# Kernel tuning notes

Measured on AMD Instinct MI355X. Metric: run time of the kernel, lower is better.

Reference implementation:

```python
import jax, jax.numpy as jnp
import numpy as np

T, H, F, E, K, C = 8192, 1024, 2048, 16, 2, 1280  # tokens, hidden, ffn, experts, top_k, capacity


def setup_inputs() -> dict:
    key = jax.random.key(0)
    ks = jax.random.split(key, 6)
    return {
        "x": jax.random.normal(ks[0], (T, H), dtype=jnp.float32),
        "w_router": jax.random.normal(ks[1], (H, E), dtype=jnp.float32) * 0.02,
        "w1": jax.random.normal(ks[2], (E, H, F), dtype=jnp.float32) * 0.02,
        "b1": jnp.zeros((E, F), dtype=jnp.float32),
        "w2": jax.random.normal(ks[3], (E, F, H), dtype=jnp.float32) * 0.02,
        "b2": jnp.zeros((E, H), dtype=jnp.float32),
    }


def reference(x, w_router, w1, b1, w2, b2):
    # ---- Router: softmax + top-k (TopKRouter) ----
    logits = x @ w_router                                  # [T, E]
    probs = jax.nn.softmax(logits, axis=-1)
    topk_p, topk_idx = jax.lax.top_k(probs, K)             # [T, K]
    topk_p = topk_p / jnp.sum(topk_p, axis=-1, keepdims=True)

    # ---- Dispatch with capacity drop (token_permutation) ----
    flat_e = topk_idx.reshape(-1)                          # [T*K] expert id per assignment
    token_ids = jnp.repeat(jnp.arange(T), K)               # [T*K]
    oh = jax.nn.one_hot(flat_e, E, dtype=jnp.int32)        # [T*K, E]
    # position of each assignment within its expert's buffer (token order)
    pos = jnp.cumsum(oh, axis=0) - oh                      # [T*K, E]
    pos = jnp.take_along_axis(pos, flat_e[:, None], axis=1)[:, 0]  # [T*K]
    keep = pos < C
    safe_pos = jnp.where(keep, pos, C)                     # dropped tokens -> dummy slot C

    dispatched = jnp.zeros((E, C + 1, H), dtype=x.dtype)
    dispatched = dispatched.at[flat_e, safe_pos].add(x[token_ids])
    disp = dispatched[:, :C, :]                            # [E, C, H]

    # ---- Grouped expert MLP (SequentialMLP: fc1 -> gelu -> fc2) ----
    h = jax.nn.gelu(jnp.einsum("ech,ehf->ecf", disp, w1) + b1[:, None, :])
    y = jnp.einsum("ecf,efh->ech", h, w2) + b2[:, None, :]  # [E, C, H]

    # ---- Combine (token_unpermutation): gather + prob-weighted sum ----
    y_pad = jnp.pad(y, ((0, 0), (0, 1), (0, 0)))            # dummy slot returns garbage, masked below
    gathered = y_pad[flat_e, safe_pos]                      # [T*K, H]
    gathered = jnp.where(keep[:, None], gathered, 0.0)
    weighted = gathered * topk_p.reshape(-1)[:, None]
    out = jax.ops.segment_sum(weighted, token_ids, num_segments=T)  # [T, H]
    return out
```

## Files before the change

### kernel.cpp

```cpp
#include <hip/hip_runtime.h>
#include <cstdint>
#include <cstddef>

#define T_TOK 8192
#define HDIM  1024
#define FDIM  2048
#define NEXP  16
#define CAP   1280

typedef __bf16 bf16x8 __attribute__((ext_vector_type(8)));
typedef float  f32x4  __attribute__((ext_vector_type(4)));

__device__ inline void gld16(const void* g, void* l) {
  __builtin_amdgcn_global_load_lds(
      (__attribute__((address_space(1))) void*)g,
      (__attribute__((address_space(3))) void*)l, 16, 0, 0);
}

__global__ __launch_bounds__(256) void router_kernel(
    const float* __restrict__ x, const float* __restrict__ wr,
    int* __restrict__ eidx, float* __restrict__ eprob) {
  int t = blockIdx.x * 4 + (threadIdx.x >> 6);
  int lane = threadIdx.x & 63;
  float acc[NEXP];
#pragma unroll
  for (int e = 0; e < NEXP; ++e) acc[e] = 0.f;
  const float4* xp = (const float4*)(x + (size_t)t * HDIM + lane * 16);
#pragma unroll
  for (int q = 0; q < 4; ++q) {
    float4 xv = xp[q];
    float xa[4] = {xv.x, xv.y, xv.z, xv.w};
#pragma unroll
    for (int ii = 0; ii < 4; ++ii) {
      int h = lane * 16 + q * 4 + ii;
      const float4* wp = (const float4*)(wr + (size_t)h * NEXP);
      float w[NEXP];
      float4 w0 = wp[0], w1 = wp[1], w2 = wp[2], w3 = wp[3];
      w[0]=w0.x; w[1]=w0.y; w[2]=w0.z; w[3]=w0.w;
      w[4]=w1.x; w[5]=w1.y; w[6]=w1.z; w[7]=w1.w;
      w[8]=w2.x; w[9]=w2.y; w[10]=w2.z; w[11]=w2.w;
      w[12]=w3.x; w[13]=w3.y; w[14]=w3.z; w[15]=w3.w;
#pragma unroll
      for (int e = 0; e < NEXP; ++e) acc[e] += xa[ii] * w[e];
    }
  }
#pragma unroll
  for (int e = 0; e < NEXP; ++e) {
#pragma unroll
    for (int s = 32; s > 0; s >>= 1) acc[e] += __shfl_xor(acc[e], s);
  }
  if (lane == 0) {
    float l0 = -1e30f, l1 = -1e30f; int i0 = 0, i1 = 0;
#pragma unroll
    for (int e = 0; e < NEXP; ++e) {
      float v = acc[e];
      if (v > l0) { l1 = l0; i1 = i0; l0 = v; i0 = e; }
      else if (v > l1) { l1 = v; i1 = e; }
    }
    float p0 = 1.f / (1.f + __expf(l1 - l0));
    eidx[t * 2 + 0] = i0; eidx[t * 2 + 1] = i1;
    eprob[t * 2 + 0] = p0; eprob[t * 2 + 1] = 1.f - p0;
  }
}

__global__ __launch_bounds__(256) void pos_kernel(
    const int* __restrict__ eidx, const float* __restrict__ eprob,
    int* __restrict__ slot_token, float* __restrict__ slot_prob) {
  __shared__ int scan[256][NEXP];
  int tid = threadIdx.x;
  int cnt[NEXP];
#pragma unroll
  for (int e = 0; e < NEXP; ++e) cnt[e] = 0;
  int base_i = tid * 64;
  const int4* ep = (const int4*)(eidx + base_i);
  for (int i = 0; i < 16; ++i) {
    int4 v = ep[i];
    cnt[v.x]++; cnt[v.y]++; cnt[v.z]++; cnt[v.w]++;
  }
#pragma unroll
  for (int e = 0; e < NEXP; ++e) scan[tid][e] = cnt[e];
  __syncthreads();
  if (tid < NEXP) {
    int run = 0;
    for (int i = 0; i < 256; ++i) { int v = scan[i][tid]; scan[i][tid] = run; run += v; }
  }
  __syncthreads();
  int basec[NEXP];
#pragma unroll
  for (int e = 0; e < NEXP; ++e) basec[e] = scan[tid][e];
  for (int i = 0; i < 64; ++i) {
    int fi = base_i + i;
    int e = eidx[fi];
    int p = basec[e]++;
    if (p < CAP) {
      slot_token[e * CAP + p] = fi >> 1;
      slot_prob[e * CAP + p] = eprob[fi];
    }
  }
}

__global__ __launch_bounds__(256) void scatter_kernel(
    const float* __restrict__ x, const int* __restrict__ slot_token,
    __bf16* __restrict__ disp) {
  int s = blockIdx.x * 4 + (threadIdx.x >> 6);
  int lane = threadIdx.x & 63;
  int tok = slot_token[s];
  __bf16 vals[16] __attribute__((aligned(16)));
  if (tok >= 0) {
    const float4* xp = (const float4*)(x + (size_t)tok * HDIM + lane * 16);
#pragma unroll
    for (int q = 0; q < 4; ++q) {
      float4 v = xp[q];
      vals[q * 4 + 0] = (__bf16)v.x; vals[q * 4 + 1] = (__bf16)v.y;
      vals[q * 4 + 2] = (__bf16)v.z; vals[q * 4 + 3] = (__bf16)v.w;
    }
  } else {
#pragma unroll
    for (int q = 0; q < 16; ++q) vals[q] = (__bf16)0.f;
  }
  uint4* dst = (uint4*)(disp + (size_t)s * HDIM + lane * 16);
  dst[0] = ((uint4*)vals)[0];
  dst[1] = ((uint4*)vals)[1];
}

__global__ __launch_bounds__(256) void transpose_cast_kernel(
    const float* __restrict__ src, __bf16* __restrict__ dst, int R, int Cc) {
  int e = blockIdx.z;
  src += (size_t)e * R * Cc;
  dst += (size_t)e * R * Cc;
  __shared__ float tile[64][65];
  int gy = blockIdx.y * 64;
  int gx = blockIdx.x * 64;
  int tid = threadIdx.x;
  int r = tid >> 4;
  int c4 = (tid & 15) * 4;
#pragma unroll
  for (int rr = 0; rr < 4; ++rr) {
    float4 v = *(const float4*)(src + (size_t)(gy + r + rr * 16) * Cc + gx + c4);
    tile[r + rr * 16][c4 + 0] = v.x;
    tile[r + rr * 16][c4 + 1] = v.y;
    tile[r + rr * 16][c4 + 2] = v.z;
    tile[r + rr * 16][c4 + 3] = v.w;
  }
  __syncthreads();
  int r2 = tid >> 2;
  int cb = (tid & 3) * 16;
  __bf16 o[16] __attribute__((aligned(16)));
#pragma unroll
  for (int i = 0; i < 16; ++i) o[i] = (__bf16)tile[cb + i][r2];
  uint4* dp = (uint4*)(dst + (size_t)(gx + r2) * R + gy + cb);
  dp[0] = ((uint4*)o)[0];
  dp[1] = ((uint4*)o)[1];
}

template <int EPI>
__global__ __launch_bounds__(256, 3) void moe_gemm_kernel(
    const __bf16* __restrict__ A, const __bf16* __restrict__ Bt,
    const float* __restrict__ bias, __bf16* __restrict__ Hout,
    const int* __restrict__ slot_token, const float* __restrict__ slot_prob,
    float* __restrict__ out, int M, int N, int Kd) {
  const int e = blockIdx.z;
  const int m0 = blockIdx.y * 128, n0 = blockIdx.x * 128;
  const __bf16* Ae = A + (size_t)e * M * Kd;
  const __bf16* Be = Bt + (size_t)e * N * Kd;
  __shared__ __bf16 lds[3 * 8192];
  const int tid = threadIdx.x, wave = tid >> 6, lane = tid & 63;
  const int quad = lane >> 4, l15 = lane & 15;
  const int wm = (wave >> 1) * 64, wn = (wave & 1) * 64;
  f32x4 acc[4][4] = {};
  const int Kb = Kd * 2;
  const int ktiles = Kd >> 5;

  const int bofs0 = wave * 2048;
  int srow[2], sgcol[2];
#pragma unroll
  for (int rr = 0; rr < 2; ++rr) {
    int lofs = bofs0 + rr * 1024 + lane * 16;
    int row = lofs >> 6;
    int chunk = (lofs >> 4) & 3;
    srow[rr] = row;
    sgcol[rr] = (chunk ^ ((row >> 1) & 3)) * 16;
  }

  auto stage = [&](int kt, int b) {
    char* dstA = (char*)lds + b * 16384;
    char* dstB = dstA + 8192;
#pragma unroll
    for (int rr = 0; rr < 2; ++rr) {
      int bofs = bofs0 + rr * 1024;
      gld16((const char*)Ae + (size_t)(m0 + srow[rr]) * Kb + kt * 64 + sgcol[rr],
            dstA + bofs);
      gld16((const char*)Be + (size_t)(n0 + srow[rr]) * Kb + kt * 64 + sgcol[rr],
            dstB + bofs);
    }
  };

  stage(0, 0);
  stage(1, 1);
  int bcur = 0, bstage = 2;
  for (int kt = 0; kt < ktiles; ++kt) {
    if (kt + 1 < ktiles) __builtin_amdgcn_s_waitcnt(0x0f74);
    else                 __builtin_amdgcn_s_waitcnt(0x0f70);
    __builtin_amdgcn_s_barrier();
    if (kt + 2 < ktiles) stage(kt + 2, bstage);
    const __bf16* La = lds + bcur * 8192;
    const __bf16* Lb = La + 4096;
    bf16x8 av[4], bv[4];
#pragma unroll
    for (int i = 0; i < 4; ++i) {
      int r = wm + i * 16 + l15;
      av[i] = *(const bf16x8*)&La[r * 32 + ((quad ^ ((r >> 1) & 3)) << 3)];
    }
#pragma unroll
    for (int j = 0; j < 4; ++j) {
      int r = wn + j * 16 + l15;
      bv[j] = *(const bf16x8*)&Lb[r * 32 + ((quad ^ ((r >> 1) & 3)) << 3)];
    }
#pragma unroll
    for (int i = 0; i < 4; ++i)
#pragma unroll
      for (int j = 0; j < 4; ++j)
        acc[i][j] = __builtin_amdgcn_mfma_f32_16x16x32_bf16(av[i], bv[j], acc[i][j], 0, 0, 0);
    bcur = (bcur == 2) ? 0 : bcur + 1;
    bstage = (bstage == 2) ? 0 : bstage + 1;
  }
  if (EPI == 1) {
    __bf16* He = Hout + (size_t)e * M * N;
#pragma unroll
    for (int i = 0; i < 4; ++i) {
#pragma unroll
      for (int r = 0; r < 4; ++r) {
        int m = m0 + wm + i * 16 + quad * 4 + r;
#pragma unroll
        for (int j = 0; j < 4; ++j) {
          int n = n0 + wn + j * 16 + l15;
          float v = acc[i][j][r] + bias[(size_t)e * N + n];
          float u = 0.7978845608028654f * (v + 0.044715f * v * v * v);
          float ex = __expf(-2.f * fabsf(u));
          float th = (1.f - ex) / (1.f + ex);
          th = copysignf(th, u);
          He[(size_t)m * N + n] = (__bf16)(0.5f * v * (1.f + th));
        }
      }
    }
  } else {
    const int* st = slot_token + e * CAP;
    const float* sp = slot_prob + e * CAP;
#pragma unroll
    for (int i = 0; i < 4; ++i) {
#pragma unroll
      for (int r = 0; r < 4; ++r) {
        int m = m0 + wm + i * 16 + quad * 4 + r;
        int tok = st[m];
        if (tok >= 0) {
          float p = sp[m];
#pragma unroll
          for (int j = 0; j < 4; ++j) {
            int n = n0 + wn + j * 16 + l15;
            float v = acc[i][j][r] + bias[(size_t)e * N + n];
            atomicAdd(out + (size_t)tok * HDIM + n, p * v);
          }
        }
      }
    }
  }
}

extern "C" void kernel_launch(void* const* d_in, const int* in_sizes, int n_in,
                              void* d_out, int out_size, void* d_ws, size_t ws_size,
                              hipStream_t stream) {
  const float* x  = (const float*)d_in[0];
  const float* wr = (const float*)d_in[1];
  const float* w1 = (const float*)d_in[2];
  const float* b1 = (const float*)d_in[3];
  const float* w2 = (const float*)d_in[4];
  const float* b2 = (const float*)d_in[5];
  float* out = (float*)d_out;

  char* ws = (char*)d_ws;
  size_t off = 0;
  __bf16* w1t = (__bf16*)(ws + off); off += (size_t)NEXP * FDIM * HDIM * 2;
  __bf16* w2t = (__bf16*)(ws + off); off += (size_t)NEXP * HDIM * FDIM * 2;
  __bf16* disp = (__bf16*)(ws + off); off += (size_t)NEXP * CAP * HDIM * 2;
  __bf16* hbuf = (__bf16*)(ws + off); off += (size_t)NEXP * CAP * FDIM * 2;
  int*   slot_token = (int*)(ws + off);  off += (size_t)NEXP * CAP * 4;
  float* slot_prob  = (float*)(ws + off); off += (size_t)NEXP * CAP * 4;
  int*   eidx  = (int*)(ws + off);  off += (size_t)T_TOK * 2 * 4;
  float* eprob = (float*)(ws + off); off += (size_t)T_TOK * 2 * 4;
  if (ws_size < off) return;

  hipMemsetAsync(slot_token, 0xFF, (size_t)NEXP * CAP * 4, stream);
  hipMemsetAsync(d_out, 0, (size_t)T_TOK * HDIM * 4, stream);

  transpose_cast_kernel<<<dim3(FDIM / 64, HDIM / 64, NEXP), 256, 0, stream>>>(w1, w1t, HDIM, FDIM);
  transpose_cast_kernel<<<dim3(HDIM / 64, FDIM / 64, NEXP), 256, 0, stream>>>(w2, w2t, FDIM, HDIM);

  router_kernel<<<T_TOK / 4, 256, 0, stream>>>(x, wr, eidx, eprob);
  pos_kernel<<<1, 256, 0, stream>>>(eidx, eprob, slot_token, slot_prob);
  scatter_kernel<<<NEXP * CAP / 4, 256, 0, stream>>>(x, slot_token, disp);

  moe_gemm_kernel<1><<<dim3(FDIM / 128, CAP / 128, NEXP), 256, 0, stream>>>(
      disp, w1t, b1, hbuf, nullptr, nullptr, nullptr, CAP, FDIM, HDIM);
  moe_gemm_kernel<2><<<dim3(HDIM / 128, CAP / 128, NEXP), 256, 0, stream>>>(
      hbuf, w2t, b2, nullptr, slot_token, slot_prob, out, CAP, HDIM, FDIM);
}
```

Measured before the change: 777.1 us.

## Enlarge expert GEMM tiles to 256x256, deepen LDS pipeline, split-K the second GEMM

```diff
diff --git a/kernel.cpp b/kernel.cpp
--- a/kernel.cpp
+++ b/kernel.cpp
@@ -153,23 +153,25 @@
   dp[1] = ((uint4*)o)[1];
 }
 
-template <int EPI>
-__global__ __launch_bounds__(256, 3) void moe_gemm_kernel(
+template <int EPI, int KSPLIT>
+__global__ __launch_bounds__(512, 2) void moe_gemm_kernel(
     const __bf16* __restrict__ A, const __bf16* __restrict__ Bt,
     const float* __restrict__ bias, __bf16* __restrict__ Hout,
     const int* __restrict__ slot_token, const float* __restrict__ slot_prob,
     float* __restrict__ out, int M, int N, int Kd) {
-  const int e = blockIdx.z;
-  const int m0 = blockIdx.y * 128, n0 = blockIdx.x * 128;
+  const int e  = blockIdx.z / KSPLIT;
+  const int ks = blockIdx.z % KSPLIT;
+  const int m0 = blockIdx.y * 256, n0 = blockIdx.x * 256;
   const __bf16* Ae = A + (size_t)e * M * Kd;
   const __bf16* Be = Bt + (size_t)e * N * Kd;
-  __shared__ __bf16 lds[3 * 8192];
+  __shared__ __bf16 lds[4 * 16384];
   const int tid = threadIdx.x, wave = tid >> 6, lane = tid & 63;
   const int quad = lane >> 4, l15 = lane & 15;
-  const int wm = (wave >> 1) * 64, wn = (wave & 1) * 64;
-  f32x4 acc[4][4] = {};
+  const int wm = (wave >> 2) * 128, wn = (wave & 3) * 64;
+  f32x4 acc[8][4] = {};
   const int Kb = Kd * 2;
-  const int ktiles = Kd >> 5;
+  const int ktiles = (Kd / KSPLIT) >> 5;
+  const int kbase = ks * (Kd / KSPLIT) * 2;
 
   const int bofs0 = wave * 2048;
   int srow[2], sgcol[2];
@@ -182,32 +184,34 @@
     sgcol[rr] = (chunk ^ ((row >> 1) & 3)) * 16;
   }
 
-  auto stage = [&](int kt, int b) {
-    char* dstA = (char*)lds + b * 16384;
-    char* dstB = dstA + 8192;
+  auto stage = [&](int kt) {
+    char* dstA = (char*)lds + (kt & 3) * 32768;
+    char* dstB = dstA + 16384;
 #pragma unroll
     for (int rr = 0; rr < 2; ++rr) {
       int bofs = bofs0 + rr * 1024;
-      gld16((const char*)Ae + (size_t)(m0 + srow[rr]) * Kb + kt * 64 + sgcol[rr],
+      gld16((const char*)Ae + (size_t)(m0 + srow[rr]) * Kb + kbase + kt * 64 + sgcol[rr],
             dstA + bofs);
-      gld16((const char*)Be + (size_t)(n0 + srow[rr]) * Kb + kt * 64 + sgcol[rr],
+      gld16((const char*)Be + (size_t)(n0 + srow[rr]) * Kb + kbase + kt * 64 + sgcol[rr],
             dstB + bofs);
     }
   };
 
-  stage(0, 0);
-  stage(1, 1);
-  int bcur = 0, bstage = 2;
+  stage(0);
+  if (ktiles > 1) stage(1);
+  if (ktiles > 2) stage(2);
   for (int kt = 0; kt < ktiles; ++kt) {
-    if (kt + 1 < ktiles) __builtin_amdgcn_s_waitcnt(0x0f74);
-    else                 __builtin_amdgcn_s_waitcnt(0x0f70);
+    int rem = ktiles - kt;
+    if (rem >= 3)      __builtin_amdgcn_s_waitcnt(0x0f78);
+    else if (rem == 2) __builtin_amdgcn_s_waitcnt(0x0f74);
+    else               __builtin_amdgcn_s_waitcnt(0x0f70);
     __builtin_amdgcn_s_barrier();
-    if (kt + 2 < ktiles) stage(kt + 2, bstage);
-    const __bf16* La = lds + bcur * 8192;
-    const __bf16* Lb = La + 4096;
-    bf16x8 av[4], bv[4];
-#pragma unroll
-    for (int i = 0; i < 4; ++i) {
+    if (kt + 3 < ktiles) stage(kt + 3);
+    const __bf16* La = lds + (kt & 3) * 16384;
+    const __bf16* Lb = La + 8192;
+    bf16x8 av[8], bv[4];
+#pragma unroll
+    for (int i = 0; i < 8; ++i) {
       int r = wm + i * 16 + l15;
       av[i] = *(const bf16x8*)&La[r * 32 + ((quad ^ ((r >> 1) & 3)) << 3)];
     }
@@ -217,24 +221,25 @@
       bv[j] = *(const bf16x8*)&Lb[r * 32 + ((quad ^ ((r >> 1) & 3)) << 3)];
     }
 #pragma unroll
-    for (int i = 0; i < 4; ++i)
+    for (int i = 0; i < 8; ++i)
 #pragma unroll
       for (int j = 0; j < 4; ++j)
         acc[i][j] = __builtin_amdgcn_mfma_f32_16x16x32_bf16(av[i], bv[j], acc[i][j], 0, 0, 0);
-    bcur = (bcur == 2) ? 0 : bcur + 1;
-    bstage = (bstage == 2) ? 0 : bstage + 1;
   }
   if (EPI == 1) {
     __bf16* He = Hout + (size_t)e * M * N;
-#pragma unroll
-    for (int i = 0; i < 4; ++i) {
+    float bj[4];
+#pragma unroll
+    for (int j = 0; j < 4; ++j) bj[j] = bias[(size_t)e * N + n0 + wn + j * 16 + l15];
+#pragma unroll
+    for (int i = 0; i < 8; ++i) {
 #pragma unroll
       for (int r = 0; r < 4; ++r) {
         int m = m0 + wm + i * 16 + quad * 4 + r;
 #pragma unroll
         for (int j = 0; j < 4; ++j) {
           int n = n0 + wn + j * 16 + l15;
-          float v = acc[i][j][r] + bias[(size_t)e * N + n];
+          float v = acc[i][j][r] + bj[j];
           float u = 0.7978845608028654f * (v + 0.044715f * v * v * v);
           float ex = __expf(-2.f * fabsf(u));
           float th = (1.f - ex) / (1.f + ex);
@@ -246,8 +251,12 @@
   } else {
     const int* st = slot_token + e * CAP;
     const float* sp = slot_prob + e * CAP;
-#pragma unroll
-    for (int i = 0; i < 4; ++i) {
+    float bj[4];
+#pragma unroll
+    for (int j = 0; j < 4; ++j)
+      bj[j] = (ks == 0) ? bias[(size_t)e * N + n0 + wn + j * 16 + l15] : 0.f;
+#pragma unroll
+    for (int i = 0; i < 8; ++i) {
 #pragma unroll
       for (int r = 0; r < 4; ++r) {
         int m = m0 + wm + i * 16 + quad * 4 + r;
@@ -257,7 +266,7 @@
 #pragma unroll
           for (int j = 0; j < 4; ++j) {
             int n = n0 + wn + j * 16 + l15;
-            float v = acc[i][j][r] + bias[(size_t)e * N + n];
+            float v = acc[i][j][r] + bj[j];
             atomicAdd(out + (size_t)tok * HDIM + n, p * v);
           }
         }
@@ -299,8 +308,8 @@
   pos_kernel<<<1, 256, 0, stream>>>(eidx, eprob, slot_token, slot_prob);
   scatter_kernel<<<NEXP * CAP / 4, 256, 0, stream>>>(x, slot_token, disp);
 
-  moe_gemm_kernel<1><<<dim3(FDIM / 128, CAP / 128, NEXP), 256, 0, stream>>>(
+  moe_gemm_kernel<1, 1><<<dim3(FDIM / 256, CAP / 256, NEXP), 512, 0, stream>>>(
       disp, w1t, b1, hbuf, nullptr, nullptr, nullptr, CAP, FDIM, HDIM);
-  moe_gemm_kernel<2><<<dim3(HDIM / 128, CAP / 128, NEXP), 256, 0, stream>>>(
+  moe_gemm_kernel<2, 2><<<dim3(HDIM / 256, CAP / 256, NEXP * 2), 512, 0, stream>>>(
       hbuf, w2t, b2, nullptr, slot_token, slot_prob, out, CAP, HDIM, FDIM);
 }
```

Measured after the change: 798.1 us. 1.03x slower.
